# Performance work log

Hardware: AMD Instinct MI355X
Metric: run time of the kernel (lower is better)

The kernel has to match this reference:

```python
import jax, jax.numpy as jnp
import numpy as np

VOCAB, CTX, EMBED, HEADS = 32000, 2048, 1024, 16


def setup_inputs() -> dict:
    key = jax.random.key(0)
    ks = jax.random.split(key, 10)
    E = EMBED
    s = 0.02
    return {
        "x": jax.random.randint(ks[0], (2, 2048), 0, VOCAB, dtype=jnp.int32),
        "tok_emb": jax.random.normal(ks[1], (VOCAB, E), jnp.float32) * s,
        "pos_emb": jax.random.normal(ks[2], (CTX, E), jnp.float32) * s,
        "qkv_w": jax.random.normal(ks[3], (E, 3 * E), jnp.float32) * s,
        "qkv_b": jnp.zeros((3 * E,), jnp.float32),
        "proj_w": jax.random.normal(ks[4], (E, E), jnp.float32) * s,
        "proj_b": jnp.zeros((E,), jnp.float32),
        "fc_w": jax.random.normal(ks[5], (E, VOCAB), jnp.float32) * s,
        "fc_b": jnp.zeros((VOCAB,), jnp.float32),
    }


def reference(x, tok_emb, pos_emb, qkv_w, qkv_b, proj_w, proj_b, fc_w, fc_b):
    B, T = x.shape
    H = HEADS
    E = tok_emb.shape[1]
    hd = E // H
    h = tok_emb[x] + pos_emb[:T][None, :, :]                      # [B,T,E]
    qkv = h @ qkv_w + qkv_b                                       # [B,T,3E]
    q, k, v = jnp.split(qkv, 3, axis=-1)
    # [B,T,E] -> [B,H,T,hd]
    q = q.reshape(B, T, H, hd).transpose(0, 2, 1, 3)
    k = k.reshape(B, T, H, hd).transpose(0, 2, 1, 3)
    v = v.reshape(B, T, H, hd).transpose(0, 2, 1, 3)
    att = jnp.einsum("bhqd,bhkd->bhqk", q, k) / jnp.sqrt(jnp.float32(hd))
    causal = jnp.tril(jnp.ones((T, T), dtype=bool))
    att = jnp.where(causal[None, None], att, jnp.float32(-jnp.inf))
    att = jax.nn.softmax(att, axis=-1)
    out = jnp.einsum("bhqk,bhkd->bhqd", att, v)                   # [B,H,T,hd]
    out = out.transpose(0, 2, 1, 3).reshape(B, T, E)
    out = out @ proj_w + proj_b
    return out @ fc_w + fc_b                                      # [B,T,VOCAB]
```

## Files before the change

### kernel.cpp

```cpp
#include <hip/hip_runtime.h>

#define BATCH 2
#define T 2048
#define E 1024
#define NH 16
#define HD 64
#define M (BATCH*T)
#define K3 (3*E)
#define VOCAB 32000

typedef __attribute__((ext_vector_type(8))) short s16x8;
typedef __attribute__((ext_vector_type(4))) short s16x4;
typedef __attribute__((ext_vector_type(4))) float f32x4;

__device__ inline unsigned short f2bf(float f) {
  union { float f; unsigned u; } x; x.f = f;
  unsigned r = x.u + 0x7fffu + ((x.u >> 16) & 1u);
  return (unsigned short)(r >> 16);
}

__device__ inline void gload16(const void* g, void* l) {
  __builtin_amdgcn_global_load_lds(
      (const __attribute__((address_space(1))) unsigned int*)g,
      (__attribute__((address_space(3))) unsigned int*)l, 16, 0, 0);
}

__global__ __launch_bounds__(256) void k_embed(const int* __restrict__ x,
    const float* __restrict__ tok, const float* __restrict__ pos,
    unsigned short* __restrict__ hb) {
  int row = blockIdx.x;
  int t = row & (T - 1);
  int tokid = x[row];
  int i = threadIdx.x;
  float4 a = ((const float4*)(tok + (size_t)tokid * E))[i];
  float4 p = ((const float4*)(pos + (size_t)t * E))[i];
  s16x4 o;
  o[0] = (short)f2bf(a.x + p.x); o[1] = (short)f2bf(a.y + p.y);
  o[2] = (short)f2bf(a.z + p.z); o[3] = (short)f2bf(a.w + p.w);
  *(s16x4*)(hb + (size_t)row * E + i * 4) = o;
}

__global__ __launch_bounds__(256) void k_wt(const float* __restrict__ W,
    unsigned short* __restrict__ Wt, int N) {
  __shared__ float tile[64][65];
  int n0 = blockIdx.x * 64, k0 = blockIdx.y * 64;
  int t = threadIdx.x;
  int kl = t >> 2, c = t & 3;
  #pragma unroll
  for (int i = 0; i < 4; i++) {
    float4 v4 = *(const float4*)(W + (size_t)(k0 + kl) * N + n0 + c * 16 + i * 4);
    tile[kl][c * 16 + i * 4 + 0] = v4.x;
    tile[kl][c * 16 + i * 4 + 1] = v4.y;
    tile[kl][c * 16 + i * 4 + 2] = v4.z;
    tile[kl][c * 16 + i * 4 + 3] = v4.w;
  }
  __syncthreads();
  #pragma unroll
  for (int j = 0; j < 2; j++) {
    int idx = t + j * 256;
    int nl = idx >> 3, kq = (idx & 7) * 8;
    s16x8 o;
    #pragma unroll
    for (int i = 0; i < 8; i++) o[i] = (short)f2bf(tile[kq + i][nl]);
    *(s16x8*)(Wt + (size_t)(n0 + nl) * 1024 + k0 + kq) = o;
  }
}

template<int MODE>
__global__ __launch_bounds__(256) void k_bgemm(
    const unsigned short* __restrict__ A, const unsigned short* __restrict__ Bt,
    const float* __restrict__ bias, float* __restrict__ C, int N,
    unsigned short* __restrict__ qo, unsigned short* __restrict__ ko,
    unsigned short* __restrict__ vo, unsigned short* __restrict__ Cb) {
  __shared__ char lds[16384];
  char* As = lds;
  char* Bs = lds + 8192;
  int tid = threadIdx.x;
  int lane = tid & 63;
  int wv = tid >> 6;
  int wm = wv >> 1, wn = wv & 1;
  int n0 = blockIdx.x * 128, m0 = blockIdx.y * 128;
  int fr = lane & 15, fq = lane >> 4;

  f32x4 acc[4][4];
  #pragma unroll
  for (int i = 0; i < 4; i++)
    #pragma unroll
    for (int j = 0; j < 4; j++) acc[i][j] = (f32x4){0.f, 0.f, 0.f, 0.f};

  int p0 = tid * 16, p1 = tid * 16 + 4096;
  int r0 = p0 >> 6, c0 = p0 & 63;
  int r1 = p1 >> 6, c1 = p1 & 63;
  int cs0 = c0 ^ (((r0 >> 1) & 3) << 4);
  int cs1 = c1 ^ (((r1 >> 1) & 3) << 4);
  const char* ga0 = (const char*)(A + (size_t)(m0 + r0) * 1024) + cs0;
  const char* ga1 = (const char*)(A + (size_t)(m0 + r1) * 1024) + cs1;
  const char* gb0 = (const char*)(Bt + (size_t)(n0 + r0) * 1024) + cs0;
  const char* gb1 = (const char*)(Bt + (size_t)(n0 + r1) * 1024) + cs1;

  int aoff[4], boff[4];
  #pragma unroll
  for (int i = 0; i < 4; i++) {
    int ra = wm * 64 + i * 16 + fr;
    aoff[i] = ra * 64 + ((fq * 16) ^ (((ra >> 1) & 3) << 4));
    int rb = wn * 64 + i * 16 + fr;
    boff[i] = rb * 64 + ((fq * 16) ^ (((rb >> 1) & 3) << 4));
  }

  for (int kb = 0; kb < 2048; kb += 64) {
    gload16(ga0 + kb, As + p0);
    gload16(ga1 + kb, As + p1);
    gload16(gb0 + kb, Bs + p0);
    gload16(gb1 + kb, Bs + p1);
    __syncthreads();
    s16x8 af[4], bfr[4];
    #pragma unroll
    for (int i = 0; i < 4; i++) af[i] = *(const s16x8*)(As + aoff[i]);
    #pragma unroll
    for (int i = 0; i < 4; i++) bfr[i] = *(const s16x8*)(Bs + boff[i]);
    #pragma unroll
    for (int mi = 0; mi < 4; mi++)
      #pragma unroll
      for (int ni = 0; ni < 4; ni++)
        acc[mi][ni] = __builtin_amdgcn_mfma_f32_16x16x32_bf16(
            af[mi], bfr[ni], acc[mi][ni], 0, 0, 0);
    __syncthreads();
  }

  if (MODE == 1) {
    #pragma unroll
    for (int mi = 0; mi < 4; mi++) {
      #pragma unroll
      for (int ni = 0; ni < 4; ni++) {
        int n = n0 + wn * 64 + ni * 16 + fr;
        int which = n >> 10;
        int e = n & (E - 1);
        int hh = e >> 6, d = e & 63;
        int mb = m0 + wm * 64 + mi * 16 + fq * 4;
        int b = mb >> 11, tt0 = mb & (T - 1);
        float bv = bias[n];
        if (which == 2) {
          s16x4 pk;
          #pragma unroll
          for (int j = 0; j < 4; j++) pk[j] = (short)f2bf(acc[mi][ni][j] + bv);
          *(s16x4*)(vo + ((size_t)(b * NH + hh) * 64 + d) * T + tt0) = pk;
        } else {
          unsigned short* dst = (which == 0) ? qo : ko;
          #pragma unroll
          for (int j = 0; j < 4; j++)
            dst[((size_t)(b * NH + hh) * T + tt0 + j) * 64 + d] =
                f2bf(acc[mi][ni][j] + bv);
        }
      }
    }
  } else {
    #pragma unroll
    for (int mi = 0; mi < 4; mi++) {
      #pragma unroll
      for (int ni = 0; ni < 4; ni++) {
        #pragma unroll
        for (int j = 0; j < 4; j++) {
          int m = m0 + wm * 64 + mi * 16 + fq * 4 + j;
          int n = n0 + wn * 64 + ni * 16 + fr;
          float val = acc[mi][ni][j] + bias[n];
          if (MODE == 0) C[(size_t)m * N + n] = val;
          else           Cb[(size_t)m * 1024 + n] = f2bf(val);
        }
      }
    }
  }
}

__global__ __launch_bounds__(512, 2) void k_fc(
    const unsigned short* __restrict__ A, const unsigned short* __restrict__ Bt,
    const float* __restrict__ bias, float* __restrict__ C) {
  __shared__ __align__(16) char lds[131072];
  int tid = threadIdx.x, lane = tid & 63, wv = tid >> 6;
  int WM = wv >> 2, WN = wv & 3;
  int fr = lane & 15, fq = lane >> 4;

  int bid = blockIdx.x;
  int wg = (bid & 7) * 250 + (bid >> 3);
  int m0 = (wg & 15) * 256;
  int n0 = (wg >> 4) * 256;

  const char* gA[4]; const char* gB[4]; int lo[4];
  #pragma unroll
  for (int j = 0; j < 4; j++) {
    int i = tid + j * 512;
    int r = i >> 3, c = i & 7;
    int cc = c ^ (r & 7);
    gA[j] = (const char*)A + ((size_t)(m0 + r) * 1024 + cc * 8) * 2;
    gB[j] = (const char*)Bt + ((size_t)(n0 + r) * 1024 + cc * 8) * 2;
    lo[j] = i * 16;
  }

  f32x4 acc[8][4];
  #pragma unroll
  for (int i = 0; i < 8; i++)
    #pragma unroll
    for (int j = 0; j < 4; j++) acc[i][j] = (f32x4){0.f, 0.f, 0.f, 0.f};

  #pragma unroll
  for (int j = 0; j < 4; j++) {
    gload16(gA[j], lds + lo[j]);
    gload16(gB[j], lds + 65536 + lo[j]);
  }
  __syncthreads();

  for (int t = 0; t < 16; t++) {
    int cur = t & 1;
    if (t + 1 < 16) {
      int kb = (t + 1) * 128;
      int nxt = cur ^ 1;
      #pragma unroll
      for (int j = 0; j < 4; j++) {
        gload16(gA[j] + kb, lds + nxt * 32768 + lo[j]);
        gload16(gB[j] + kb, lds + 65536 + nxt * 32768 + lo[j]);
      }
    }
    const char* As = lds + cur * 32768;
    const char* Bs = lds + 65536 + cur * 32768;
    #pragma unroll
    for (int kh = 0; kh < 2; kh++) {
      s16x8 af[8], bf[4];
      #pragma unroll
      for (int mi = 0; mi < 8; mi++) {
        int r = WM * 128 + mi * 16 + fr;
        af[mi] = *(const s16x8*)(As + r * 128 + (((kh * 4 + fq) ^ (r & 7)) << 4));
      }
      #pragma unroll
      for (int ni = 0; ni < 4; ni++) {
        int r = WN * 64 + ni * 16 + fr;
        bf[ni] = *(const s16x8*)(Bs + r * 128 + (((kh * 4 + fq) ^ (r & 7)) << 4));
      }
      __builtin_amdgcn_s_setprio(1);
      #pragma unroll
      for (int mi = 0; mi < 8; mi++)
        #pragma unroll
        for (int ni = 0; ni < 4; ni++)
          acc[mi][ni] = __builtin_amdgcn_mfma_f32_16x16x32_bf16(
              af[mi], bf[ni], acc[mi][ni], 0, 0, 0);
      __builtin_amdgcn_s_setprio(0);
    }
    __syncthreads();
  }

  #pragma unroll
  for (int mi = 0; mi < 8; mi++) {
    #pragma unroll
    for (int ni = 0; ni < 4; ni++) {
      int n = n0 + WN * 64 + ni * 16 + fr;
      float bv = bias[n];
      #pragma unroll
      for (int j = 0; j < 4; j++) {
        int m = m0 + WM * 128 + mi * 16 + fq * 4 + j;
        C[(size_t)m * VOCAB + n] = acc[mi][ni][j] + bv;
      }
    }
  }
}

#define BM 128
#define BN 128
#define BKF 32
#define LDT (BM + 4)
__global__ __launch_bounds__(256) void k_gemm32(
    const float* __restrict__ A, const float* __restrict__ Bw,
    const float* __restrict__ bias, float* __restrict__ C, int N) {
  __shared__ float As[BKF * LDT];
  __shared__ float Bs[BKF * LDT];
  int tid = threadIdx.x;
  int tx = tid & 15, ty = tid >> 4;
  int n0 = blockIdx.x * BN;
  int m0 = blockIdx.y * BM;
  float acc[8][8];
  #pragma unroll
  for (int i = 0; i < 8; i++)
    #pragma unroll
    for (int j = 0; j < 8; j++) acc[i][j] = 0.f;
  for (int k0 = 0; k0 < E; k0 += BKF) {
    #pragma unroll
    for (int i = 0; i < 4; i++) {
      int f = i * 256 + tid;
      int ml = f >> 3, c4 = f & 7;
      float4 va = *(const float4*)(A + (size_t)(m0 + ml) * E + k0 + c4 * 4);
      As[(c4 * 4 + 0) * LDT + ml] = va.x;
      As[(c4 * 4 + 1) * LDT + ml] = va.y;
      As[(c4 * 4 + 2) * LDT + ml] = va.z;
      As[(c4 * 4 + 3) * LDT + ml] = va.w;
    }
    #pragma unroll
    for (int i = 0; i < 4; i++) {
      int f = i * 256 + tid;
      int kk = f >> 5, c4 = f & 31;
      float4 vb = *(const float4*)(Bw + (size_t)(k0 + kk) * N + n0 + c4 * 4);
      *(float4*)(Bs + kk * LDT + c4 * 4) = vb;
    }
    __syncthreads();
    #pragma unroll
    for (int kk = 0; kk < BKF; kk++) {
      const float4* ar = (const float4*)(As + kk * LDT);
      const float4* br = (const float4*)(Bs + kk * LDT);
      float4 a0 = ar[ty * 2], a1 = ar[ty * 2 + 1];
      float4 b0 = br[tx * 2], b1 = br[tx * 2 + 1];
      float av[8] = {a0.x, a0.y, a0.z, a0.w, a1.x, a1.y, a1.z, a1.w};
      float bvv[8] = {b0.x, b0.y, b0.z, b0.w, b1.x, b1.y, b1.z, b1.w};
      #pragma unroll
      for (int i = 0; i < 8; i++)
        #pragma unroll
        for (int j = 0; j < 8; j++)
          acc[i][j] = fmaf(av[i], bvv[j], acc[i][j]);
    }
    __syncthreads();
  }
  int mbase = m0 + ty * 8;
  int nbase = n0 + tx * 8;
  #pragma unroll
  for (int i = 0; i < 8; i++) {
    float* crow = C + (size_t)(mbase + i) * N + nbase;
    #pragma unroll
    for (int j = 0; j < 8; j++) crow[j] = acc[i][j] + bias[nbase + j];
  }
}

__global__ __launch_bounds__(256) void k_attn2(
    const unsigned short* __restrict__ qb, const unsigned short* __restrict__ kb,
    const unsigned short* __restrict__ vtb, unsigned short* __restrict__ o) {
  __shared__ char lds[40960];
  int qt = 31 - (int)blockIdx.x;
  int bh = blockIdx.y;
  int b = bh >> 4, hh = bh & 15;
  int tid = threadIdx.x, lane = tid & 63, wv = tid >> 6;
  int fr = lane & 15, fq = lane >> 4;
  int q0 = qt * 64;
  int qw = q0 + wv * 16;
  const unsigned short* Qg = qb + ((size_t)bh * T + qw) * 64;
  const char* Kg = (const char*)(kb + (size_t)bh * T * 64);
  const char* Vg = (const char*)(vtb + (size_t)bh * 64 * T);
  char* Pl = lds + 32768 + wv * 2048;

  s16x8 qf[2];
  qf[0] = *(const s16x8*)(Qg + (size_t)fr * 64 + fq * 8);
  qf[1] = *(const s16x8*)(Qg + (size_t)fr * 64 + 32 + fq * 8);

  f32x4 po[4];
  #pragma unroll
  for (int i = 0; i < 4; i++) po[i] = (f32x4){0.f, 0.f, 0.f, 0.f};
  float mrow[4], lrow[4];
  #pragma unroll
  for (int j = 0; j < 4; j++) { mrow[j] = -1e30f; lrow[j] = 0.f; }

  int ntiles = qt + 1;
  int i0 = tid, i1 = tid + 256;
  int sr0 = i0 >> 3, sc0 = ((i0 & 7) ^ (sr0 & 7)) << 4;
  int sr1 = i1 >> 3, sc1 = ((i1 & 7) ^ (sr1 & 7)) << 4;

  {
    gload16(Kg + (size_t)sr0 * 128 + sc0, lds + i0 * 16);
    gload16(Kg + (size_t)sr1 * 128 + sc1, lds + i1 * 16);
    gload16(Vg + (size_t)sr0 * (T * 2) + sc0, lds + 16384 + i0 * 16);
    gload16(Vg + (size_t)sr1 * (T * 2) + sc1, lds + 16384 + i1 * 16);
  }
  __syncthreads();
  int cur = 0;

  for (int kt = 0; kt < ntiles; kt++) {
    int kv0 = kt * 64;
    if (kt + 1 < ntiles) {
      size_t kvn = (size_t)(kv0 + 64);
      char* kd = lds + (cur ^ 1) * 8192;
      char* vd = lds + 16384 + (cur ^ 1) * 8192;
      gload16(Kg + (kvn + sr0) * 128 + sc0, kd + i0 * 16);
      gload16(Kg + (kvn + sr1) * 128 + sc1, kd + i1 * 16);
      gload16(Vg + (size_t)sr0 * (T * 2) + kvn * 2 + sc0, vd + i0 * 16);
      gload16(Vg + (size_t)sr1 * (T * 2) + kvn * 2 + sc1, vd + i1 * 16);
    }
    const char* Kt = lds + cur * 8192;
    const char* Vt = lds + 16384 + cur * 8192;

    f32x4 s[4];
    #pragma unroll
    for (int ni = 0; ni < 4; ni++) {
      s[ni] = (f32x4){0.f, 0.f, 0.f, 0.f};
      int r = ni * 16 + fr;
      s16x8 kf0 = *(const s16x8*)(Kt + r * 128 + ((fq ^ (r & 7)) << 4));
      s16x8 kf1 = *(const s16x8*)(Kt + r * 128 + (((4 + fq) ^ (r & 7)) << 4));
      s[ni] = __builtin_amdgcn_mfma_f32_16x16x32_bf16(qf[0], kf0, s[ni], 0, 0, 0);
      s[ni] = __builtin_amdgcn_mfma_f32_16x16x32_bf16(qf[1], kf1, s[ni], 0, 0, 0);
    }

    bool needm = (kv0 + 63 > qw);
    #pragma unroll
    for (int jj = 0; jj < 4; jj++) {
      int row = qw + fq * 4 + jj;
      float tm = -1e30f;
      #pragma unroll
      for (int ni = 0; ni < 4; ni++) {
        float val = s[ni][jj] * 0.125f;
        if (needm) { int col = kv0 + ni * 16 + fr; if (col > row) val = -1e30f; }
        s[ni][jj] = val;
        tm = fmaxf(tm, val);
      }
      #pragma unroll
      for (int mk = 1; mk < 16; mk <<= 1) tm = fmaxf(tm, __shfl_xor(tm, mk));
      float nm = fmaxf(mrow[jj], tm);
      float corr = __expf(mrow[jj] - nm);
      mrow[jj] = nm;
      #pragma unroll
      for (int ni = 0; ni < 4; ni++) po[ni][jj] *= corr;
      float rs = 0.f;
      #pragma unroll
      for (int ni = 0; ni < 4; ni++) {
        float pv = __expf(s[ni][jj] - nm);
        s[ni][jj] = pv;
        rs += pv;
      }
      #pragma unroll
      for (int mk = 1; mk < 16; mk <<= 1) rs += __shfl_xor(rs, mk);
      lrow[jj] = lrow[jj] * corr + rs;
    }

    #pragma unroll
    for (int ni = 0; ni < 4; ni++) {
      int col = ni * 16 + fr;
      #pragma unroll
      for (int jj = 0; jj < 4; jj++) {
        int qq = fq * 4 + jj;
        *(unsigned short*)(Pl + qq * 128 + (((col >> 3) ^ (qq & 7)) << 4) +
                           (col & 7) * 2) = f2bf(s[ni][jj]);
      }
    }
    asm volatile("s_waitcnt lgkmcnt(0)" ::: "memory");

    s16x8 pa0 = *(const s16x8*)(Pl + fr * 128 + ((fq ^ (fr & 7)) << 4));
    s16x8 pa1 = *(const s16x8*)(Pl + fr * 128 + (((4 + fq) ^ (fr & 7)) << 4));
    #pragma unroll
    for (int ni = 0; ni < 4; ni++) {
      int r = ni * 16 + fr;
      s16x8 vf0 = *(const s16x8*)(Vt + r * 128 + ((fq ^ (r & 7)) << 4));
      s16x8 vf1 = *(const s16x8*)(Vt + r * 128 + (((4 + fq) ^ (r & 7)) << 4));
      po[ni] = __builtin_amdgcn_mfma_f32_16x16x32_bf16(pa0, vf0, po[ni], 0, 0, 0);
      po[ni] = __builtin_amdgcn_mfma_f32_16x16x32_bf16(pa1, vf1, po[ni], 0, 0, 0);
    }
    __syncthreads();
    cur ^= 1;
  }

  #pragma unroll
  for (int jj = 0; jj < 4; jj++) {
    float inv = 1.f / lrow[jj];
    int row = qw + fq * 4 + jj;
    unsigned short* orow = o + ((size_t)(b * T + row)) * E + hh * 64;
    #pragma unroll
    for (int ni = 0; ni < 4; ni++)
      orow[ni * 16 + fr] = f2bf(po[ni][jj] * inv);
  }
}

extern "C" void kernel_launch(void* const* d_in, const int* in_sizes, int n_in,
                              void* d_out, int out_size, void* d_ws, size_t ws_size,
                              hipStream_t stream) {
  const int*   x      = (const int*)d_in[0];
  const float* tok    = (const float*)d_in[1];
  const float* pos    = (const float*)d_in[2];
  const float* qkv_w  = (const float*)d_in[3];
  const float* qkv_b  = (const float*)d_in[4];
  const float* proj_w = (const float*)d_in[5];
  const float* proj_b = (const float*)d_in[6];
  const float* fc_w   = (const float*)d_in[7];
  const float* fc_b   = (const float*)d_in[8];
  float* out = (float*)d_out;
  float* ws  = (float*)d_ws;

  unsigned short* hb      = (unsigned short*)out;
  unsigned short* qkv_wt  = (unsigned short*)(out + 2097152);
  unsigned short* qbuf    = (unsigned short*)(out + 3670016);
  unsigned short* kbuf    = (unsigned short*)(out + 5767168);
  unsigned short* vtbuf   = (unsigned short*)(out + 7864320);
  unsigned short* aob     = (unsigned short*)(out + 9961472);
  unsigned short* proj_wt = (unsigned short*)(out + 12058624);

  const size_t WS_FAST = (size_t)(2097152 + 16384000) * 4;

  k_embed<<<M, 256, 0, stream>>>(x, tok, pos, hb);
  k_wt<<<dim3(K3 / 64, 16), 256, 0, stream>>>(qkv_w, qkv_wt, K3);
  k_bgemm<1><<<dim3(K3 / 128, M / 128), 256, 0, stream>>>(
      hb, qkv_wt, qkv_b, nullptr, K3, qbuf, kbuf, vtbuf, nullptr);
  k_attn2<<<dim3(32, 32), 256, 0, stream>>>(qbuf, kbuf, vtbuf, aob);
  k_wt<<<dim3(E / 64, 16), 256, 0, stream>>>(proj_w, proj_wt, E);

  if (ws_size >= WS_FAST) {
    unsigned short* h2b   = (unsigned short*)ws;
    unsigned short* fc_wt = (unsigned short*)(ws + 2097152);
    k_bgemm<2><<<dim3(E / 128, M / 128), 256, 0, stream>>>(
        aob, proj_wt, proj_b, nullptr, E, nullptr, nullptr, nullptr, h2b);
    k_wt<<<dim3(VOCAB / 64, 16), 256, 0, stream>>>(fc_w, fc_wt, VOCAB);
    k_fc<<<dim3((M / 256) * (VOCAB / 256)), 512, 0, stream>>>(
        h2b, fc_wt, fc_b, out);
  } else {
    float* h2 = ws;
    k_bgemm<0><<<dim3(E / 128, M / 128), 256, 0, stream>>>(
        aob, proj_wt, proj_b, h2, E, nullptr, nullptr, nullptr, nullptr);
    k_gemm32<<<dim3(VOCAB / BN, M / BM), 256, 0, stream>>>(
        h2, fc_w, fc_b, out, VOCAB);
  }
}
```

Measured before the change: 585.6 us.

## Switch FC GEMM to 4-stage pipelined K=64 tiles with manual waitcnt

The vocab projection GEMM now uses 64-wide K steps with a 4-deep LDS ring buffer, issuing loads three stages ahead instead of double-buffering 128-wide K tiles. It replaces __syncthreads with explicit vmcnt/lgkmcnt waits plus s_barrier so async global-to-LDS loads stay in flight across iterations. The XOR swizzle is dropped for a plain 64-byte row layout, which may bring back LDS bank conflicts on the fragment reads. It also doubles the number of barriers per K.

```diff
diff --git a/kernel.cpp b/kernel.cpp
--- a/kernel.cpp
+++ b/kernel.cpp
@@ -184,16 +184,12 @@
   int m0 = (wg & 15) * 256;
   int n0 = (wg >> 4) * 256;
 
-  const char* gA[4]; const char* gB[4]; int lo[4];
-  #pragma unroll
-  for (int j = 0; j < 4; j++) {
-    int i = tid + j * 512;
-    int r = i >> 3, c = i & 7;
-    int cc = c ^ (r & 7);
-    gA[j] = (const char*)A + ((size_t)(m0 + r) * 1024 + cc * 8) * 2;
-    gB[j] = (const char*)Bt + ((size_t)(n0 + r) * 1024 + cc * 8) * 2;
-    lo[j] = i * 16;
-  }
+  int i0 = tid, i1 = tid + 512;
+  const char* gA0 = (const char*)A + (size_t)(m0 + (i0 >> 2)) * 2048 + (i0 & 3) * 16;
+  const char* gA1 = (const char*)A + (size_t)(m0 + (i1 >> 2)) * 2048 + (i1 & 3) * 16;
+  const char* gB0 = (const char*)Bt + (size_t)(n0 + (i0 >> 2)) * 2048 + (i0 & 3) * 16;
+  const char* gB1 = (const char*)Bt + (size_t)(n0 + (i1 >> 2)) * 2048 + (i1 & 3) * 16;
+  int l0 = i0 * 16, l1 = i1 * 16;
 
   f32x4 acc[8][4];
   #pragma unroll
@@ -201,50 +197,44 @@
     #pragma unroll
     for (int j = 0; j < 4; j++) acc[i][j] = (f32x4){0.f, 0.f, 0.f, 0.f};
 
-  #pragma unroll
-  for (int j = 0; j < 4; j++) {
-    gload16(gA[j], lds + lo[j]);
-    gload16(gB[j], lds + 65536 + lo[j]);
-  }
-  __syncthreads();
-
-  for (int t = 0; t < 16; t++) {
-    int cur = t & 1;
-    if (t + 1 < 16) {
-      int kb = (t + 1) * 128;
-      int nxt = cur ^ 1;
-      #pragma unroll
-      for (int j = 0; j < 4; j++) {
-        gload16(gA[j] + kb, lds + nxt * 32768 + lo[j]);
-        gload16(gB[j] + kb, lds + 65536 + nxt * 32768 + lo[j]);
-      }
-    }
-    const char* As = lds + cur * 32768;
-    const char* Bs = lds + 65536 + cur * 32768;
-    #pragma unroll
-    for (int kh = 0; kh < 2; kh++) {
-      s16x8 af[8], bf[4];
-      #pragma unroll
-      for (int mi = 0; mi < 8; mi++) {
-        int r = WM * 128 + mi * 16 + fr;
-        af[mi] = *(const s16x8*)(As + r * 128 + (((kh * 4 + fq) ^ (r & 7)) << 4));
-      }
-      #pragma unroll
-      for (int ni = 0; ni < 4; ni++) {
-        int r = WN * 64 + ni * 16 + fr;
-        bf[ni] = *(const s16x8*)(Bs + r * 128 + (((kh * 4 + fq) ^ (r & 7)) << 4));
-      }
-      __builtin_amdgcn_s_setprio(1);
-      #pragma unroll
-      for (int mi = 0; mi < 8; mi++)
-        #pragma unroll
-        for (int ni = 0; ni < 4; ni++)
-          acc[mi][ni] = __builtin_amdgcn_mfma_f32_16x16x32_bf16(
-              af[mi], bf[ni], acc[mi][ni], 0, 0, 0);
-      __builtin_amdgcn_s_setprio(0);
-    }
-    __syncthreads();
-  }
+#define STAGE(t) do { char* s_ = lds + ((t) & 3) * 32768; int kb_ = (t) * 64; \
+    gload16(gA0 + kb_, s_ + l0);         gload16(gA1 + kb_, s_ + l1);         \
+    gload16(gB0 + kb_, s_ + 16384 + l0); gload16(gB1 + kb_, s_ + 16384 + l1); \
+  } while (0)
+
+  STAGE(0); STAGE(1); STAGE(2);
+  asm volatile("s_waitcnt vmcnt(8)" ::: "memory");
+  __builtin_amdgcn_sched_barrier(0);
+  __builtin_amdgcn_s_barrier();
+  __builtin_amdgcn_sched_barrier(0);
+
+  for (int t = 0; t < 32; t++) {
+    if (t + 3 < 32) STAGE(t + 3);
+    const char* As = lds + (t & 3) * 32768;
+    const char* Bs = As + 16384;
+    s16x8 af[8], bf[4];
+    #pragma unroll
+    for (int mi = 0; mi < 8; mi++)
+      af[mi] = *(const s16x8*)(As + (WM * 128 + mi * 16 + fr) * 64 + fq * 16);
+    #pragma unroll
+    for (int ni = 0; ni < 4; ni++)
+      bf[ni] = *(const s16x8*)(Bs + (WN * 64 + ni * 16 + fr) * 64 + fq * 16);
+    __builtin_amdgcn_s_setprio(1);
+    #pragma unroll
+    for (int mi = 0; mi < 8; mi++)
+      #pragma unroll
+      for (int ni = 0; ni < 4; ni++)
+        acc[mi][ni] = __builtin_amdgcn_mfma_f32_16x16x32_bf16(
+            af[mi], bf[ni], acc[mi][ni], 0, 0, 0);
+    __builtin_amdgcn_s_setprio(0);
+    if (t < 29)       asm volatile("s_waitcnt lgkmcnt(0) vmcnt(8)" ::: "memory");
+    else if (t == 29) asm volatile("s_waitcnt lgkmcnt(0) vmcnt(4)" ::: "memory");
+    else              asm volatile("s_waitcnt lgkmcnt(0) vmcnt(0)" ::: "memory");
+    __builtin_amdgcn_sched_barrier(0);
+    __builtin_amdgcn_s_barrier();
+    __builtin_amdgcn_sched_barrier(0);
+  }
+#undef STAGE
 
   #pragma unroll
   for (int mi = 0; mi < 8; mi++) {
```

After: 617.5 us. 5.4% more time.

## Process 128 query rows per attention block and add lazy softmax rescaling

Applied to the files above, without the earlier changes.

The attention kernel now gives each wave two 16-row query groups, so a block covers 128 queries and each K/V tile loaded into LDS is reused twice. This halves the grid and the total K/V traffic. It also skips the running-max correction unless the new max exceeds the old one by more than 8, which saves exp and multiply work. The cost is more register pressure, fewer blocks for occupancy, and coarser causal load balance. The thresholded rescale keeps the result exact, since the sum is corrected consistently, but values can grow up to e^8 before a rescale.

```diff
diff --git a/kernel.cpp b/kernel.cpp
--- a/kernel.cpp
+++ b/kernel.cpp
@@ -328,30 +328,36 @@
     const unsigned short* __restrict__ qb, const unsigned short* __restrict__ kb,
     const unsigned short* __restrict__ vtb, unsigned short* __restrict__ o) {
   __shared__ char lds[40960];
-  int qt = 31 - (int)blockIdx.x;
+  int qt = 15 - (int)blockIdx.x;
   int bh = blockIdx.y;
   int b = bh >> 4, hh = bh & 15;
   int tid = threadIdx.x, lane = tid & 63, wv = tid >> 6;
   int fr = lane & 15, fq = lane >> 4;
-  int q0 = qt * 64;
-  int qw = q0 + wv * 16;
-  const unsigned short* Qg = qb + ((size_t)bh * T + qw) * 64;
+  int q0 = qt * 128;
+  int qw0 = q0 + wv * 32;
   const char* Kg = (const char*)(kb + (size_t)bh * T * 64);
   const char* Vg = (const char*)(vtb + (size_t)bh * 64 * T);
   char* Pl = lds + 32768 + wv * 2048;
 
-  s16x8 qf[2];
-  qf[0] = *(const s16x8*)(Qg + (size_t)fr * 64 + fq * 8);
-  qf[1] = *(const s16x8*)(Qg + (size_t)fr * 64 + 32 + fq * 8);
-
-  f32x4 po[4];
-  #pragma unroll
-  for (int i = 0; i < 4; i++) po[i] = (f32x4){0.f, 0.f, 0.f, 0.f};
-  float mrow[4], lrow[4];
-  #pragma unroll
-  for (int j = 0; j < 4; j++) { mrow[j] = -1e30f; lrow[j] = 0.f; }
-
-  int ntiles = qt + 1;
+  s16x8 qf[2][2];
+  #pragma unroll
+  for (int g = 0; g < 2; g++) {
+    const unsigned short* Qg = qb + ((size_t)bh * T + qw0 + g * 16) * 64;
+    qf[g][0] = *(const s16x8*)(Qg + (size_t)fr * 64 + fq * 8);
+    qf[g][1] = *(const s16x8*)(Qg + (size_t)fr * 64 + 32 + fq * 8);
+  }
+
+  f32x4 po[2][4];
+  float mrow[2][4], lrow[2][4];
+  #pragma unroll
+  for (int g = 0; g < 2; g++)
+    #pragma unroll
+    for (int j = 0; j < 4; j++) {
+      po[g][j] = (f32x4){0.f, 0.f, 0.f, 0.f};
+      mrow[g][j] = -1e30f; lrow[g][j] = 0.f;
+    }
+
+  int ntiles = qt * 2 + 2;
   int i0 = tid, i1 = tid + 256;
   int sr0 = i0 >> 3, sc0 = ((i0 & 7) ^ (sr0 & 7)) << 4;
   int sr1 = i1 >> 3, sc1 = ((i1 & 7) ^ (sr1 & 7)) << 4;
@@ -379,83 +385,94 @@
     const char* Kt = lds + cur * 8192;
     const char* Vt = lds + 16384 + cur * 8192;
 
-    f32x4 s[4];
-    #pragma unroll
-    for (int ni = 0; ni < 4; ni++) {
-      s[ni] = (f32x4){0.f, 0.f, 0.f, 0.f};
-      int r = ni * 16 + fr;
-      s16x8 kf0 = *(const s16x8*)(Kt + r * 128 + ((fq ^ (r & 7)) << 4));
-      s16x8 kf1 = *(const s16x8*)(Kt + r * 128 + (((4 + fq) ^ (r & 7)) << 4));
-      s[ni] = __builtin_amdgcn_mfma_f32_16x16x32_bf16(qf[0], kf0, s[ni], 0, 0, 0);
-      s[ni] = __builtin_amdgcn_mfma_f32_16x16x32_bf16(qf[1], kf1, s[ni], 0, 0, 0);
-    }
-
-    bool needm = (kv0 + 63 > qw);
-    #pragma unroll
-    for (int jj = 0; jj < 4; jj++) {
-      int row = qw + fq * 4 + jj;
-      float tm = -1e30f;
+    #pragma unroll
+    for (int g = 0; g < 2; g++) {
+      int qw = qw0 + g * 16;
+      f32x4 s[4];
       #pragma unroll
       for (int ni = 0; ni < 4; ni++) {
-        float val = s[ni][jj] * 0.125f;
-        if (needm) { int col = kv0 + ni * 16 + fr; if (col > row) val = -1e30f; }
-        s[ni][jj] = val;
-        tm = fmaxf(tm, val);
-      }
-      #pragma unroll
-      for (int mk = 1; mk < 16; mk <<= 1) tm = fmaxf(tm, __shfl_xor(tm, mk));
-      float nm = fmaxf(mrow[jj], tm);
-      float corr = __expf(mrow[jj] - nm);
-      mrow[jj] = nm;
-      #pragma unroll
-      for (int ni = 0; ni < 4; ni++) po[ni][jj] *= corr;
-      float rs = 0.f;
+        s[ni] = (f32x4){0.f, 0.f, 0.f, 0.f};
+        int r = ni * 16 + fr;
+        s16x8 kf0 = *(const s16x8*)(Kt + r * 128 + ((fq ^ (r & 7)) << 4));
+        s16x8 kf1 = *(const s16x8*)(Kt + r * 128 + (((4 + fq) ^ (r & 7)) << 4));
+        s[ni] = __builtin_amdgcn_mfma_f32_16x16x32_bf16(qf[g][0], kf0, s[ni], 0, 0, 0);
+        s[ni] = __builtin_amdgcn_mfma_f32_16x16x32_bf16(qf[g][1], kf1, s[ni], 0, 0, 0);
+      }
+
+      bool needm = (kv0 + 63 > qw);
+      #pragma unroll
+      for (int jj = 0; jj < 4; jj++) {
+        int row = qw + fq * 4 + jj;
+        float tm = -1e30f;
+        #pragma unroll
+        for (int ni = 0; ni < 4; ni++) {
+          float val = s[ni][jj] * 0.125f;
+          if (needm) { int col = kv0 + ni * 16 + fr; if (col > row) val = -1e30f; }
+          s[ni][jj] = val;
+          tm = fmaxf(tm, val);
+        }
+        #pragma unroll
+        for (int mk = 1; mk < 16; mk <<= 1) tm = fmaxf(tm, __shfl_xor(tm, mk));
+        if (__any(tm > mrow[g][jj] + 8.f)) {
+          float nm = fmaxf(mrow[g][jj], tm);
+          float corr = __expf(mrow[g][jj] - nm);
+          mrow[g][jj] = nm;
+          #pragma unroll
+          for (int ni = 0; ni < 4; ni++) po[g][ni][jj] *= corr;
+          lrow[g][jj] *= corr;
+        }
+        float mref = mrow[g][jj];
+        float rs = 0.f;
+        #pragma unroll
+        for (int ni = 0; ni < 4; ni++) {
+          float pv = __expf(s[ni][jj] - mref);
+          s[ni][jj] = pv;
+          rs += pv;
+        }
+        #pragma unroll
+        for (int mk = 1; mk < 16; mk <<= 1) rs += __shfl_xor(rs, mk);
+        lrow[g][jj] += rs;
+      }
+
+      asm volatile("s_waitcnt lgkmcnt(0)" ::: "memory");
       #pragma unroll
       for (int ni = 0; ni < 4; ni++) {
-        float pv = __expf(s[ni][jj] - nm);
-        s[ni][jj] = pv;
-        rs += pv;
-      }
-      #pragma unroll
-      for (int mk = 1; mk < 16; mk <<= 1) rs += __shfl_xor(rs, mk);
-      lrow[jj] = lrow[jj] * corr + rs;
-    }
-
-    #pragma unroll
-    for (int ni = 0; ni < 4; ni++) {
-      int col = ni * 16 + fr;
-      #pragma unroll
-      for (int jj = 0; jj < 4; jj++) {
-        int qq = fq * 4 + jj;
-        *(unsigned short*)(Pl + qq * 128 + (((col >> 3) ^ (qq & 7)) << 4) +
-                           (col & 7) * 2) = f2bf(s[ni][jj]);
-      }
-    }
-    asm volatile("s_waitcnt lgkmcnt(0)" ::: "memory");
-
-    s16x8 pa0 = *(const s16x8*)(Pl + fr * 128 + ((fq ^ (fr & 7)) << 4));
-    s16x8 pa1 = *(const s16x8*)(Pl + fr * 128 + (((4 + fq) ^ (fr & 7)) << 4));
-    #pragma unroll
-    for (int ni = 0; ni < 4; ni++) {
-      int r = ni * 16 + fr;
-      s16x8 vf0 = *(const s16x8*)(Vt + r * 128 + ((fq ^ (r & 7)) << 4));
-      s16x8 vf1 = *(const s16x8*)(Vt + r * 128 + (((4 + fq) ^ (r & 7)) << 4));
-      po[ni] = __builtin_amdgcn_mfma_f32_16x16x32_bf16(pa0, vf0, po[ni], 0, 0, 0);
-      po[ni] = __builtin_amdgcn_mfma_f32_16x16x32_bf16(pa1, vf1, po[ni], 0, 0, 0);
+        int col = ni * 16 + fr;
+        #pragma unroll
+        for (int jj = 0; jj < 4; jj++) {
+          int qq = fq * 4 + jj;
+          *(unsigned short*)(Pl + qq * 128 + (((col >> 3) ^ (qq & 7)) << 4) +
+                             (col & 7) * 2) = f2bf(s[ni][jj]);
+        }
+      }
+      asm volatile("s_waitcnt lgkmcnt(0)" ::: "memory");
+
+      s16x8 pa0 = *(const s16x8*)(Pl + fr * 128 + ((fq ^ (fr & 7)) << 4));
+      s16x8 pa1 = *(const s16x8*)(Pl + fr * 128 + (((4 + fq) ^ (fr & 7)) << 4));
+      #pragma unroll
+      for (int ni = 0; ni < 4; ni++) {
+        int r = ni * 16 + fr;
+        s16x8 vf0 = *(const s16x8*)(Vt + r * 128 + ((fq ^ (r & 7)) << 4));
+        s16x8 vf1 = *(const s16x8*)(Vt + r * 128 + (((4 + fq) ^ (r & 7)) << 4));
+        po[g][ni] = __builtin_amdgcn_mfma_f32_16x16x32_bf16(pa0, vf0, po[g][ni], 0, 0, 0);
+        po[g][ni] = __builtin_amdgcn_mfma_f32_16x16x32_bf16(pa1, vf1, po[g][ni], 0, 0, 0);
+      }
     }
     __syncthreads();
     cur ^= 1;
   }
 
   #pragma unroll
-  for (int jj = 0; jj < 4; jj++) {
-    float inv = 1.f / lrow[jj];
-    int row = qw + fq * 4 + jj;
-    unsigned short* orow = o + ((size_t)(b * T + row)) * E + hh * 64;
-    #pragma unroll
-    for (int ni = 0; ni < 4; ni++)
-      orow[ni * 16 + fr] = f2bf(po[ni][jj] * inv);
-  }
+  for (int g = 0; g < 2; g++)
+    #pragma unroll
+    for (int jj = 0; jj < 4; jj++) {
+      float inv = 1.f / lrow[g][jj];
+      int row = qw0 + g * 16 + fq * 4 + jj;
+      unsigned short* orow = o + ((size_t)(b * T + row)) * E + hh * 64;
+      #pragma unroll
+      for (int ni = 0; ni < 4; ni++)
+        orow[ni * 16 + fr] = f2bf(po[g][ni][jj] * inv);
+    }
 }
 
 extern "C" void kernel_launch(void* const* d_in, const int* in_sizes, int n_in,
@@ -487,7 +504,7 @@
   k_wt<<<dim3(K3 / 64, 16), 256, 0, stream>>>(qkv_w, qkv_wt, K3);
   k_bgemm<1><<<dim3(K3 / 128, M / 128), 256, 0, stream>>>(
       hb, qkv_wt, qkv_b, nullptr, K3, qbuf, kbuf, vtbuf, nullptr);
-  k_attn2<<<dim3(32, 32), 256, 0, stream>>>(qbuf, kbuf, vtbuf, aob);
+  k_attn2<<<dim3(16, 32), 256, 0, stream>>>(qbuf, kbuf, vtbuf, aob);
   k_wt<<<dim3(E / 64, 16), 256, 0, stream>>>(proj_w, proj_wt, E);
 
   if (ws_size >= WS_FAST) {
```

Result: no change. 582.8 us (-0.5%).
